# Kernel tuning notes

Hardware: AMD Instinct MI355X
Metric: run time of the kernel (lower is better)

The kernel has to match this reference:

```python
import jax, jax.numpy as jnp
import numpy as np

B, N, T, M, D, H = 2, 2048, 8, 256, 1024, 16
HD = D // H
EPS = 1e-5


def setup_inputs() -> dict:
    key = jax.random.key(0)
    ks = jax.random.split(key, 12)
    text_tokens = jax.random.normal(ks[0], (B, N, D), dtype=jnp.float32)
    media = jax.random.normal(ks[1], (B, T, M, D), dtype=jnp.float32)
    # exactly T media markers, evenly spaced, first at position 0 so no
    # fully-masked softmax row (matches well-formed usage of the module)
    loc = np.zeros((B, N), dtype=bool)
    loc[:, (np.arange(T) * (N // T))] = True
    media_locations = jnp.asarray(loc)
    s = 0.02
    return {
        "text_tokens": text_tokens,
        "media": media,
        "media_locations": media_locations,
        "ln_gamma": jnp.ones((D,), jnp.float32),
        "ln_beta": jnp.zeros((D,), jnp.float32),
        "wq": jax.random.normal(ks[2], (D, D), jnp.float32) * s,
        "wk": jax.random.normal(ks[3], (D, D), jnp.float32) * s,
        "wv": jax.random.normal(ks[4], (D, D), jnp.float32) * s,
        "bq": jnp.zeros((D,), jnp.float32),
        "bk": jnp.zeros((D,), jnp.float32),
        "bv": jnp.zeros((D,), jnp.float32),
        "w_out": jax.random.normal(ks[5], (D, D), jnp.float32) * s,
        "b_out": jnp.zeros((D,), jnp.float32),
    }


def _layernorm(x, gamma, beta):
    mu = jnp.mean(x, axis=-1, keepdims=True)
    var = jnp.mean(jnp.square(x - mu), axis=-1, keepdims=True)
    return (x - mu) * jax.lax.rsqrt(var + EPS) * gamma + beta


def reference(text_tokens, media, media_locations, ln_gamma, ln_beta,
              wq, wk, wv, bq, bk, bv, w_out, b_out):
    b, t, m, d = media.shape
    n = text_tokens.shape[1]
    h, hd = H, HD

    x = _layernorm(text_tokens, ln_gamma, ln_beta)          # [b,n,d]
    kv = media.reshape(b, t * m, d)                          # [b,tm,d]

    q = (x @ wq + bq).reshape(b, n, h, hd)
    k = (kv @ wk + bk).reshape(b, t * m, h, hd)
    v = (kv @ wv + bv).reshape(b, t * m, h, hd)

    scale = 1.0 / jnp.sqrt(jnp.asarray(hd, jnp.float32))
    scores = jnp.einsum('bnhk,bshk->bhns', q, k) * scale     # [b,h,n,tm]

    # media-locality mask: text token attends only to its immediately
    # preceding media frame (cumsum of media_locations == frame index)
    text_cumsum = jnp.cumsum(media_locations.astype(jnp.int32), axis=-1)  # [b,n]
    media_nums = jnp.repeat(jnp.arange(1, t + 1, dtype=jnp.int32), m)     # [tm]
    allowed = text_cumsum[:, :, None] == media_nums[None, None, :]        # [b,n,tm]
    scores = jnp.where(allowed[:, None, :, :], scores, -jnp.inf)

    attn = jax.nn.softmax(scores, axis=-1)                   # [b,h,n,tm]
    out = jnp.einsum('bhns,bshk->bnhk', attn, v).reshape(b, n, d)
    return out @ w_out + b_out
```

## Files before the change

### kernel.cpp

```cpp
#include <hip/hip_runtime.h>
#include <hip/hip_fp16.h>


typedef _Float16 h8 __attribute__((ext_vector_type(8)));
typedef _Float16 h4 __attribute__((ext_vector_type(4)));
typedef float f4 __attribute__((ext_vector_type(4)));

#define DI __device__ __forceinline__

DI void gload16(const void* g, void* l) {
  __builtin_amdgcn_global_load_lds((const __attribute__((address_space(1))) unsigned int*)g,
                                   (__attribute__((address_space(3))) unsigned int*)l, 16, 0, 0);
}

__global__ __launch_bounds__(256) void prep_kernel(
    const float* __restrict__ x, const float* __restrict__ gamma, const float* __restrict__ beta,
    _Float16* __restrict__ xh,
    const float* __restrict__ media, _Float16* __restrict__ kvh,
    const float* __restrict__ W0, const float* __restrict__ W1,
    const float* __restrict__ W2, const float* __restrict__ W3, _Float16* __restrict__ Wt,
    const int* __restrict__ locs, int* __restrict__ cnt, int* __restrict__ qlist) {
  int bid = blockIdx.x;
  int tid = threadIdx.x;
  if (bid < 4096) {
    int row = bid;
    const f4* xr = (const f4*)(x + (size_t)row * 1024);
    f4 v = xr[tid];
    float s = v[0] + v[1] + v[2] + v[3];
    float ss = v[0]*v[0] + v[1]*v[1] + v[2]*v[2] + v[3]*v[3];
    #pragma unroll
    for (int m = 1; m < 64; m <<= 1) { s += __shfl_xor(s, m); ss += __shfl_xor(ss, m); }
    __shared__ float red[8];
    int wid = tid >> 6, lane = tid & 63;
    if (lane == 0) { red[wid] = s; red[4 + wid] = ss; }
    __syncthreads();
    s = red[0] + red[1] + red[2] + red[3];
    ss = red[4] + red[5] + red[6] + red[7];
    float mean = s * (1.0f / 1024.0f);
    float var = ss * (1.0f / 1024.0f) - mean * mean;
    float rs = rsqrtf(var + 1e-5f);
    f4 g = ((const f4*)gamma)[tid], be = ((const f4*)beta)[tid];
    h4 o;
    #pragma unroll
    for (int j = 0; j < 4; ++j) o[j] = (_Float16)((v[j] - mean) * rs * g[j] + be[j]);
    ((h4*)(xh + (size_t)row * 1024))[tid] = o;
  } else if (bid < 8192) {
    int i = (bid - 4096) * 256 + tid;
    f4 v = ((const f4*)media)[i];
    h4 o;
    #pragma unroll
    for (int j = 0; j < 4; ++j) o[j] = (_Float16)v[j];
    ((h4*)kvh)[i] = o;
  } else if (bid < 9216) {
    int sec = bid - 8192;
    int z = sec >> 8, r = sec & 255;
    const float* W = z == 0 ? W0 : z == 1 ? W1 : z == 2 ? W2 : W3;
    _Float16* out = Wt + (size_t)z * 1024 * 1024;
    __shared__ float tileF[64][65];
    int i0 = (r & 15) * 64, o0 = (r >> 4) * 64;
    #pragma unroll
    for (int p = 0; p < 4; ++p) {
      int ir = p * 16 + (tid >> 4);
      f4 v = *(const f4*)&W[(size_t)(i0 + ir) * 1024 + o0 + (tid & 15) * 4];
      #pragma unroll
      for (int j = 0; j < 4; ++j) tileF[ir][(tid & 15) * 4 + j] = v[j];
    }
    __syncthreads();
    #pragma unroll
    for (int p = 0; p < 2; ++p) {
      int orow = p * 32 + (tid >> 3);
      h8 v;
      #pragma unroll
      for (int j = 0; j < 8; ++j) v[j] = (_Float16)tileF[(tid & 7) * 8 + j][orow];
      *(h8*)&out[(size_t)(o0 + orow) * 1024 + i0 + (tid & 7) * 8] = v;
    }
  } else {
    int b = bid - 9216;
    __shared__ int lcnt[8];
    if (tid < 8) lcnt[tid] = 0;
    __syncthreads();
    if (tid < 64) {
      int lane = tid;
      int run = 0; int v[32];
      #pragma unroll
      for (int i = 0; i < 32; ++i) { run += locs[b * 2048 + lane * 32 + i]; v[i] = run; }
      int incl = run;
      #pragma unroll
      for (int d = 1; d < 64; d <<= 1) { int t = __shfl_up(incl, d); if (lane >= d) incl += t; }
      int excl = incl - run;
      #pragma unroll
      for (int i = 0; i < 32; ++i) {
        int c = excl + v[i];
        if (c >= 1 && c <= 8) {
          int pos = atomicAdd(&lcnt[c - 1], 1);
          qlist[(b * 8 + (c - 1)) * 2048 + pos] = lane * 32 + i;
        }
      }
    }
    __syncthreads();
    if (tid < 8) cnt[b * 8 + tid] = lcnt[tid];
  }
}

struct GemmDesc { const _Float16* A; const _Float16* Bt; const float* bias; void* C; int mode; };
struct GemmBatch { GemmDesc d[3]; };

__global__ __launch_bounds__(512) void gemm128(GemmBatch gb) {
  GemmDesc g = gb.d[blockIdx.z];
  int id = blockIdx.y * 8 + blockIdx.x;
  int id2 = (id & 7) * 32 + (id >> 3);
  int row0 = (id2 >> 3) * 128, col0 = (id2 & 7) * 128;
  __shared__ alignas(16) _Float16 As[128 * 64];
  __shared__ alignas(16) _Float16 Bs[128 * 64];
  int tid = threadIdx.x, lane = tid & 63, wid = tid >> 6;
  int wr = wid >> 2, wc = wid & 3;
  f4 acc[4][2] = {};
  int r0s = tid >> 3, c0s = tid & 7;
  int cg0 = c0s ^ (r0s & 7);
  const _Float16* gA0 = g.A + (size_t)(row0 + r0s) * 1024 + cg0 * 8;
  const _Float16* gA1 = gA0 + (size_t)64 * 1024;
  const _Float16* gB0 = g.Bt + (size_t)(col0 + r0s) * 1024 + cg0 * 8;
  const _Float16* gB1 = gB0 + (size_t)64 * 1024;
  #pragma unroll 1
  for (int kt = 0; kt < 16; ++kt) {
    __syncthreads();
    gload16(gA0 + kt * 64, (void*)&As[wid * 512]);
    gload16(gA1 + kt * 64, (void*)&As[4096 + wid * 512]);
    gload16(gB0 + kt * 64, (void*)&Bs[wid * 512]);
    gload16(gB1 + kt * 64, (void*)&Bs[4096 + wid * 512]);
    __syncthreads();
    h8 af[2][4], bf[2][2];
    #pragma unroll
    for (int kk = 0; kk < 2; ++kk) {
      #pragma unroll
      for (int m = 0; m < 4; ++m) {
        int r = wr * 64 + m * 16 + (lane & 15);
        int c = ((lane >> 4) + kk * 4) ^ (r & 7);
        af[kk][m] = *(const h8*)&As[r * 64 + c * 8];
      }
      #pragma unroll
      for (int n = 0; n < 2; ++n) {
        int r = wc * 32 + n * 16 + (lane & 15);
        int c = ((lane >> 4) + kk * 4) ^ (r & 7);
        bf[kk][n] = *(const h8*)&Bs[r * 64 + c * 8];
      }
    }
    #pragma unroll
    for (int kk = 0; kk < 2; ++kk)
      #pragma unroll
      for (int m = 0; m < 4; ++m)
        #pragma unroll
        for (int n = 0; n < 2; ++n)
          acc[m][n] = __builtin_amdgcn_mfma_f32_16x16x32_f16(af[kk][m], bf[kk][n], acc[m][n], 0, 0, 0);
  }
  int colb = col0 + wc * 32;
  float bias_v[2];
  #pragma unroll
  for (int n = 0; n < 2; ++n) bias_v[n] = g.bias[colb + n * 16 + (lane & 15)];
  #pragma unroll
  for (int m = 0; m < 4; ++m) {
    int row = row0 + wr * 64 + m * 16 + (lane >> 4) * 4;
    #pragma unroll
    for (int n = 0; n < 2; ++n) {
      int col = colb + n * 16 + (lane & 15);
      if (g.mode == 0) {
        _Float16* C = (_Float16*)g.C;
        #pragma unroll
        for (int j = 0; j < 4; ++j)
          C[(size_t)(row + j) * 1024 + col] = (_Float16)(acc[m][n][j] + bias_v[n]);
      } else {
        _Float16* C = (_Float16*)g.C;
        h4 pk;
        #pragma unroll
        for (int j = 0; j < 4; ++j) pk[j] = (_Float16)(acc[m][n][j] + bias_v[n]);
        size_t vrow = (size_t)((row >> 11) * 1024 + col);
        *(h4*)&C[vrow * 2048 + (row & 2047)] = pk;
      }
    }
  }
}

__global__ __launch_bounds__(512) void gemm_out(const _Float16* __restrict__ A,
    const _Float16* __restrict__ Bt, const float* __restrict__ bias, float* __restrict__ C) {
  int id = blockIdx.y * 8 + blockIdx.x;
  int id2 = (id & 7) * 64 + (id >> 3);
  int row0 = (id2 >> 3) * 64, col0 = (id2 & 7) * 128;
  __shared__ alignas(16) _Float16 As[64 * 64];
  __shared__ alignas(16) _Float16 Bs[128 * 64];
  int tid = threadIdx.x, lane = tid & 63, wid = tid >> 6;
  int wr = wid >> 2, wc = wid & 3;
  f4 acc[2][2] = {};
  int rs = tid >> 3, c0s = tid & 7;
  int cg = c0s ^ (rs & 7);
  const _Float16* gA  = A  + (size_t)(row0 + rs) * 1024 + cg * 8;
  const _Float16* gB0 = Bt + (size_t)(col0 + rs) * 1024 + cg * 8;
  const _Float16* gB1 = gB0 + (size_t)64 * 1024;
  #pragma unroll 1
  for (int kt = 0; kt < 16; ++kt) {
    __syncthreads();
    gload16(gA  + kt * 64, (void*)&As[wid * 512]);
    gload16(gB0 + kt * 64, (void*)&Bs[wid * 512]);
    gload16(gB1 + kt * 64, (void*)&Bs[4096 + wid * 512]);
    __syncthreads();
    #pragma unroll
    for (int kk = 0; kk < 2; ++kk) {
      h8 a[2], b[2];
      #pragma unroll
      for (int m = 0; m < 2; ++m) {
        int r = wr * 32 + m * 16 + (lane & 15);
        int c = ((lane >> 4) + kk * 4) ^ (r & 7);
        a[m] = *(const h8*)&As[r * 64 + c * 8];
      }
      #pragma unroll
      for (int n = 0; n < 2; ++n) {
        int r = wc * 32 + n * 16 + (lane & 15);
        int c = ((lane >> 4) + kk * 4) ^ (r & 7);
        b[n] = *(const h8*)&Bs[r * 64 + c * 8];
      }
      #pragma unroll
      for (int m = 0; m < 2; ++m)
        #pragma unroll
        for (int n = 0; n < 2; ++n)
          acc[m][n] = __builtin_amdgcn_mfma_f32_16x16x32_f16(a[m], b[n], acc[m][n], 0, 0, 0);
    }
  }
  int colb = col0 + wc * 32;
  float bias_v[2];
  #pragma unroll
  for (int n = 0; n < 2; ++n) bias_v[n] = bias[colb + n * 16 + (lane & 15)];
  #pragma unroll
  for (int m = 0; m < 2; ++m) {
    int row = row0 + wr * 32 + m * 16 + (lane >> 4) * 4;
    #pragma unroll
    for (int n = 0; n < 2; ++n) {
      int col = colb + n * 16 + (lane & 15);
      #pragma unroll
      for (int j = 0; j < 4; ++j)
        C[(size_t)(row + j) * 1024 + col] = acc[m][n][j] + bias_v[n];
    }
  }
}

__global__ __launch_bounds__(512) void attn_kernel(const _Float16* __restrict__ Qg,
    const _Float16* __restrict__ Kg, const _Float16* __restrict__ Vtg,
    const int* __restrict__ cnt, const int* __restrict__ qlist, _Float16* __restrict__ Og) {
  int h = blockIdx.x, f = blockIdx.y, b = blockIdx.z;
  __shared__ alignas(16) _Float16 Kl[256 * 64];
  __shared__ alignas(16) _Float16 Vl[64 * 256];
  __shared__ alignas(16) _Float16 Sl[8 * 16 * 256];
  int tid = threadIdx.x;
  for (int idx = tid; idx < 2048; idx += 512) {
    int r = idx >> 3, c = idx & 7;
    h8 v = *(const h8*)&Kg[((size_t)(b * 2048 + f * 256 + r)) * 1024 + h * 64 + c * 8];
    *(h8*)&Kl[r * 64 + ((c ^ (r & 7)) * 8)] = v;
  }
  for (int idx = tid; idx < 2048; idx += 512) {
    int d = idx >> 5, cc = idx & 31;
    h8 v = *(const h8*)&Vtg[((size_t)(b * 1024 + h * 64 + d)) * 2048 + f * 256 + cc * 8];
    *(h8*)&Vl[d * 256 + ((cc ^ (d & 7)) * 8)] = v;
  }
  __syncthreads();
  int nq = cnt[b * 8 + f];
  int lane = tid & 63, wid = tid >> 6;
  const int* ql = qlist + (b * 8 + f) * 2048;
  _Float16* Sw = &Sl[wid * 4096];
  for (int st = wid; st * 16 < nq; st += 8) {
    int qbase = st * 16;
    int nv = nq - qbase; if (nv > 16) nv = 16;
    int li = lane & 15; if (li > nv - 1) li = nv - 1;
    int qrow = b * 2048 + ql[qbase + li];
    h8 aq0 = *(const h8*)&Qg[(size_t)qrow * 1024 + h * 64 + (lane >> 4) * 8];
    h8 aq1 = *(const h8*)&Qg[(size_t)qrow * 1024 + h * 64 + 32 + (lane >> 4) * 8];
    f4 s[16];
    #pragma unroll
    for (int kt = 0; kt < 16; ++kt) {
      int key = kt * 16 + (lane & 15);
      int cb0 = lane >> 4;
      h8 bk0 = *(const h8*)&Kl[key * 64 + ((cb0 ^ (key & 7)) * 8)];
      h8 bk1 = *(const h8*)&Kl[key * 64 + (((cb0 + 4) ^ (key & 7)) * 8)];
      f4 z = {0.f, 0.f, 0.f, 0.f};
      s[kt] = __builtin_amdgcn_mfma_f32_16x16x32_f16(aq0, bk0, z, 0, 0, 0);
      s[kt] = __builtin_amdgcn_mfma_f32_16x16x32_f16(aq1, bk1, s[kt], 0, 0, 0);
    }
    float mx[4], sm[4];
    #pragma unroll
    for (int j = 0; j < 4; ++j) {
      float m = s[0][j];
      #pragma unroll
      for (int kt = 1; kt < 16; ++kt) m = fmaxf(m, s[kt][j]);
      #pragma unroll
      for (int d = 1; d < 16; d <<= 1) m = fmaxf(m, __shfl_xor(m, d));
      mx[j] = m; sm[j] = 0.f;
    }
    #pragma unroll
    for (int kt = 0; kt < 16; ++kt) {
      int keyb = kt * 16 + (lane & 15);
      int cbk = keyb >> 3, wi = keyb & 7;
      #pragma unroll
      for (int j = 0; j < 4; ++j) {
        float p = __expf((s[kt][j] - mx[j]) * 0.125f);
        sm[j] += p;
        int q = (lane >> 4) * 4 + j;
        Sw[q * 256 + ((cbk ^ (q & 7)) * 8) + wi] = (_Float16)p;
      }
    }
    #pragma unroll
    for (int j = 0; j < 4; ++j) {
      float x = sm[j];
      #pragma unroll
      for (int d = 1; d < 16; d <<= 1) x += __shfl_xor(x, d);
      sm[j] = x;
    }
    f4 o[4] = {};
    #pragma unroll
    for (int c32 = 0; c32 < 8; ++c32) {
      int qa = lane & 15;
      int cba = c32 * 4 + (lane >> 4);
      h8 pa = *(const h8*)&Sw[qa * 256 + ((cba ^ (qa & 7)) * 8)];
      #pragma unroll
      for (int dt = 0; dt < 4; ++dt) {
        int dd = dt * 16 + (lane & 15);
        h8 bv_ = *(const h8*)&Vl[dd * 256 + ((cba ^ (dd & 7)) * 8)];
        o[dt] = __builtin_amdgcn_mfma_f32_16x16x32_f16(pa, bv_, o[dt], 0, 0, 0);
      }
    }
    #pragma unroll
    for (int j = 0; j < 4; ++j) {
      int q = (lane >> 4) * 4 + j;
      if (q < nv) {
        int qr = __shfl(qrow, q);
        float inv = 1.0f / sm[j];
        #pragma unroll
        for (int dt = 0; dt < 4; ++dt)
          Og[(size_t)qr * 1024 + h * 64 + dt * 16 + (lane & 15)] = (_Float16)(o[dt][j] * inv);
      }
    }
  }
}

extern "C" void kernel_launch(void* const* d_in, const int* in_sizes, int n_in,
                              void* d_out, int out_size, void* d_ws, size_t ws_size,
                              hipStream_t stream) {
  const float* text  = (const float*)d_in[0];
  const float* media = (const float*)d_in[1];
  const int*   locs  = (const int*)d_in[2];
  const float* gamma = (const float*)d_in[3];
  const float* beta  = (const float*)d_in[4];
  const float* wq = (const float*)d_in[5];
  const float* wk = (const float*)d_in[6];
  const float* wv = (const float*)d_in[7];
  const float* bq = (const float*)d_in[8];
  const float* bk = (const float*)d_in[9];
  const float* bv = (const float*)d_in[10];
  const float* wo = (const float*)d_in[11];
  const float* bo = (const float*)d_in[12];

  char* ws = (char*)d_ws;
  size_t off = 0;
  auto take = [&](size_t bytes) { void* p = ws + off; off += (bytes + 255) & ~(size_t)255; return p; };
  _Float16* xh  = (_Float16*)take((size_t)4096 * 1024 * 2);
  _Float16* kvh = (_Float16*)take((size_t)4096 * 1024 * 2);
  _Float16* wt  = (_Float16*)take((size_t)4 * 1024 * 1024 * 2);
  _Float16* Qm  = (_Float16*)take((size_t)4096 * 1024 * 2);
  _Float16* Km  = (_Float16*)take((size_t)4096 * 1024 * 2);
  _Float16* Vt  = (_Float16*)take((size_t)2048 * 2048 * 2);
  _Float16* Om  = (_Float16*)take((size_t)4096 * 1024 * 2);
  int* cnt   = (int*)take(64 * sizeof(int));
  int* qlist = (int*)take((size_t)2 * 8 * 2048 * sizeof(int));

  prep_kernel<<<9218, 256, 0, stream>>>(text, gamma, beta, xh, media, kvh,
                                        wq, wk, wv, wo, wt, locs, cnt, qlist);

  GemmBatch gb;
  gb.d[0] = { xh,  wt,                       bq, (void*)Qm, 0 };
  gb.d[1] = { kvh, wt + (size_t)1 * 1048576, bk, (void*)Km, 0 };
  gb.d[2] = { kvh, wt + (size_t)2 * 1048576, bv, (void*)Vt, 2 };
  gemm128<<<dim3(8, 32, 3), 512, 0, stream>>>(gb);

  attn_kernel<<<dim3(16, 8, 2), 512, 0, stream>>>(Qm, Km, Vt, cnt, qlist, Om);

  gemm_out<<<dim3(8, 64), 512, 0, stream>>>(Om, wt + (size_t)3 * 1048576, bo, (float*)d_out);
}
```

Before: 173.1 us.

## Use 4 waves with 64x64 warp tiles in QKV GEMM

Restructures the QKV projection GEMM from 8 waves, each computing a 64x32 tile, to 4 waves, each computing a 64x64 tile. Every wave now issues 16 MFMAs per k-substep and reuses its A and B fragments across more outputs, so LDS reads per MFMA drop. Launch bounds are set to allow 3 blocks per CU. The cost is more accumulator registers per thread and fewer waves per block to hide load latency, and each thread now issues twice as many global-to-LDS loads.

```diff
diff --git a/kernel.cpp b/kernel.cpp
--- a/kernel.cpp
+++ b/kernel.cpp
@@ -105,7 +105,7 @@
 struct GemmDesc { const _Float16* A; const _Float16* Bt; const float* bias; void* C; int mode; };
 struct GemmBatch { GemmDesc d[3]; };
 
-__global__ __launch_bounds__(512) void gemm128(GemmBatch gb) {
+__global__ __launch_bounds__(256, 3) void gemm128(GemmBatch gb) {
   GemmDesc g = gb.d[blockIdx.z];
   int id = blockIdx.y * 8 + blockIdx.x;
   int id2 = (id & 7) * 32 + (id >> 3);
@@ -113,55 +113,57 @@
   __shared__ alignas(16) _Float16 As[128 * 64];
   __shared__ alignas(16) _Float16 Bs[128 * 64];
   int tid = threadIdx.x, lane = tid & 63, wid = tid >> 6;
-  int wr = wid >> 2, wc = wid & 3;
-  f4 acc[4][2] = {};
-  int r0s = tid >> 3, c0s = tid & 7;
-  int cg0 = c0s ^ (r0s & 7);
-  const _Float16* gA0 = g.A + (size_t)(row0 + r0s) * 1024 + cg0 * 8;
-  const _Float16* gA1 = gA0 + (size_t)64 * 1024;
-  const _Float16* gB0 = g.Bt + (size_t)(col0 + r0s) * 1024 + cg0 * 8;
-  const _Float16* gB1 = gB0 + (size_t)64 * 1024;
+  int wr = wid >> 1, wc = wid & 1;
+  f4 acc[4][4] = {};
+  int rs = tid >> 3, cs = tid & 7;
+  const _Float16* gA[4]; const _Float16* gB[4];
+  #pragma unroll
+  for (int p = 0; p < 4; ++p) {
+    int rp = p * 32 + rs;
+    int cg = cs ^ (rp & 7);
+    gA[p] = g.A  + (size_t)(row0 + rp) * 1024 + cg * 8;
+    gB[p] = g.Bt + (size_t)(col0 + rp) * 1024 + cg * 8;
+  }
   #pragma unroll 1
   for (int kt = 0; kt < 16; ++kt) {
     __syncthreads();
-    gload16(gA0 + kt * 64, (void*)&As[wid * 512]);
-    gload16(gA1 + kt * 64, (void*)&As[4096 + wid * 512]);
-    gload16(gB0 + kt * 64, (void*)&Bs[wid * 512]);
-    gload16(gB1 + kt * 64, (void*)&Bs[4096 + wid * 512]);
-    __syncthreads();
-    h8 af[2][4], bf[2][2];
+    #pragma unroll
+    for (int p = 0; p < 4; ++p) {
+      gload16(gA[p] + kt * 64, (void*)&As[p * 2048 + wid * 512]);
+      gload16(gB[p] + kt * 64, (void*)&Bs[p * 2048 + wid * 512]);
+    }
+    __syncthreads();
     #pragma unroll
     for (int kk = 0; kk < 2; ++kk) {
+      h8 af[4], bf[4];
       #pragma unroll
       for (int m = 0; m < 4; ++m) {
         int r = wr * 64 + m * 16 + (lane & 15);
         int c = ((lane >> 4) + kk * 4) ^ (r & 7);
-        af[kk][m] = *(const h8*)&As[r * 64 + c * 8];
-      }
-      #pragma unroll
-      for (int n = 0; n < 2; ++n) {
-        int r = wc * 32 + n * 16 + (lane & 15);
+        af[m] = *(const h8*)&As[r * 64 + c * 8];
+      }
+      #pragma unroll
+      for (int n = 0; n < 4; ++n) {
+        int r = wc * 64 + n * 16 + (lane & 15);
         int c = ((lane >> 4) + kk * 4) ^ (r & 7);
-        bf[kk][n] = *(const h8*)&Bs[r * 64 + c * 8];
-      }
-    }
-    #pragma unroll
-    for (int kk = 0; kk < 2; ++kk)
+        bf[n] = *(const h8*)&Bs[r * 64 + c * 8];
+      }
       #pragma unroll
       for (int m = 0; m < 4; ++m)
         #pragma unroll
-        for (int n = 0; n < 2; ++n)
-          acc[m][n] = __builtin_amdgcn_mfma_f32_16x16x32_f16(af[kk][m], bf[kk][n], acc[m][n], 0, 0, 0);
-  }
-  int colb = col0 + wc * 32;
-  float bias_v[2];
-  #pragma unroll
-  for (int n = 0; n < 2; ++n) bias_v[n] = g.bias[colb + n * 16 + (lane & 15)];
+        for (int n = 0; n < 4; ++n)
+          acc[m][n] = __builtin_amdgcn_mfma_f32_16x16x32_f16(af[m], bf[n], acc[m][n], 0, 0, 0);
+    }
+  }
+  int colb = col0 + wc * 64;
+  float bias_v[4];
+  #pragma unroll
+  for (int n = 0; n < 4; ++n) bias_v[n] = g.bias[colb + n * 16 + (lane & 15)];
   #pragma unroll
   for (int m = 0; m < 4; ++m) {
     int row = row0 + wr * 64 + m * 16 + (lane >> 4) * 4;
     #pragma unroll
-    for (int n = 0; n < 2; ++n) {
+    for (int n = 0; n < 4; ++n) {
       int col = colb + n * 16 + (lane & 15);
       if (g.mode == 0) {
         _Float16* C = (_Float16*)g.C;
@@ -375,7 +377,7 @@
   gb.d[0] = { xh,  wt,                       bq, (void*)Qm, 0 };
   gb.d[1] = { kvh, wt + (size_t)1 * 1048576, bk, (void*)Km, 0 };
   gb.d[2] = { kvh, wt + (size_t)2 * 1048576, bv, (void*)Vt, 2 };
-  gemm128<<<dim3(8, 32, 3), 512, 0, stream>>>(gb);
+  gemm128<<<dim3(8, 32, 3), 256, 0, stream>>>(gb);
 
   attn_kernel<<<dim3(16, 8, 2), 512, 0, stream>>>(Qm, Km, Vt, cnt, qlist, Om);
 
```

New measurement: 179.1 us. +3.4%, slower.
